# Performance work log

Hardware: AMD Instinct MI355X
Metric: run time of the kernel (lower is better)

Reference implementation:

```python
import jax, jax.numpy as jnp
import numpy as np

N_FREQS = 6  # PositionEmbedding N_freqs when embedding=='pe'

def _pe(x):
    freqs = (2.0 ** jnp.arange(N_FREQS)).astype(x.dtype)
    fx = x * freqs  # [B,Q,N_FREQS]
    sc = jnp.stack([jnp.sin(fx), jnp.cos(fx)], axis=-1).reshape(fx.shape[0], fx.shape[1], 2 * N_FREQS)
    return jnp.concatenate([x, sc], axis=-1)

def _mlp(h, W1, b1, W2, b2, W3, b3):
    h = jax.nn.relu(h @ W1 + b1)
    h = jax.nn.relu(h @ W2 + b2)
    return h @ W3 + b3

def setup_inputs() -> dict:
    key = jax.random.key(0)
    B, Q, N, D, H = 4, 65536, 8192, 16, 128
    ks = jax.random.split(key, 6)
    coord = jax.random.uniform(ks[0], (B, Q, 1), minval=-1.0, maxval=1.0, dtype=jnp.float32)
    latent = jax.random.normal(ks[1], (B, N, D), dtype=jnp.float32)
    in_dim = (1 + 2 * N_FREQS) + 3 * D  # pe(rel_coord) ++ unfolded feat = 13 + 48 = 61
    def init(k, shp, fan):
        return (jax.random.normal(k, shp, dtype=jnp.float32) / np.float32(np.sqrt(fan)))
    W1 = init(ks[2], (in_dim, H), in_dim); b1 = jnp.zeros((H,), jnp.float32)
    W2 = init(ks[3], (H, H), H);          b2 = jnp.zeros((H,), jnp.float32)
    W3 = init(ks[4], (H, 1), H);          b3 = jnp.zeros((1,), jnp.float32)
    return dict(coord=coord, latent=latent, W1=W1, b1=b1, W2=W2, b2=b2, W3=W3, b3=b3)

def reference(coord, latent, W1, b1, W2, b2, W3, b3):
    B, Q, _ = coord.shape
    N = latent.shape[1]
    # feat_unfold: concat shifted-prev / self / shifted-next along feature dim -> [B,N,3D]
    prev = jnp.concatenate([latent[:, :1], latent[:, :-1]], axis=1)
    nxt = jnp.concatenate([latent[:, 1:], latent[:, -1:]], axis=1)
    feat = jnp.concatenate([prev, latent, nxt], axis=-1)
    # make_coord grid: cell centers in [-1,1]
    grid = (-1.0 + (2.0 * jnp.arange(N, dtype=coord.dtype) + 1.0) / N)
    rx = 1.0 / N           # 2/num_latents/2
    eps_shift = 1e-6
    preds, areas = [], []
    for vx in (-2.0, 0.0):  # eval path vx_lst
        c = jnp.clip(coord + vx * rx + eps_shift, -1.0 + 1e-6, 1.0 - 1e-6)
        idx = jnp.clip(jnp.searchsorted(grid, c[..., 0]), 0, N - 1)  # [B,Q]
        q_coord = grid[idx][..., None]                               # [B,Q,1]
        q_feat = jnp.take_along_axis(feat, idx[..., None], axis=1)   # [B,Q,3D]
        rel = (coord - q_coord) * N                                  # scaled rel coord
        area = jnp.abs(rel[..., 0]) + 1e-9                           # [B,Q]
        inp = jnp.concatenate([_pe(rel), q_feat], axis=-1)           # [B,Q,61]
        preds.append(_mlp(inp, W1, b1, W2, b2, W3, b3))              # [B,Q,1]
        areas.append(area)
    tot = areas[0] + areas[1]
    # local_ensemble: swap areas before weighting
    ret = preds[0] * (areas[1] / tot)[..., None] + preds[1] * (areas[0] / tot)[..., None]
    return ret
```

## Files before the change

kernel.cpp:

```cpp
#include <hip/hip_runtime.h>
#include <hip/hip_bf16.h>

typedef short s8v __attribute__((ext_vector_type(8)));
typedef float f4v __attribute__((ext_vector_type(4)));

__device__ __forceinline__ unsigned short f2bf(float x) {
  unsigned u = __builtin_bit_cast(unsigned, x);
  u += 0x7fffu + ((u >> 16) & 1u);
  return (unsigned short)(u >> 16);
}
__device__ __forceinline__ unsigned pk2(float a, float b) {
  return (unsigned)f2bf(a) | ((unsigned)f2bf(b) << 16);
}

__global__ void prep_kernel(const float* __restrict__ W1, const float* __restrict__ b1,
                            const float* __restrict__ W2, unsigned short* __restrict__ wsW) {
  int e = blockIdx.x * 256 + threadIdx.x;
  if (e < 8192) {
    int frag = e >> 9, rem = e & 511, lane = rem >> 3, j = rem & 7;
    int h = frag >> 1, ks = frag & 1;
    int q4 = lane >> 4, l15 = lane & 15;
    int k = ks * 32 + q4 * 8 + j;
    int n = h * 16 + l15;
    float v;
    if (k < 13) v = W1[k * 128 + n];
    else if (k == 13) v = b1[n];
    else if (k < 16) v = 0.0f;
    else v = W1[(k - 3) * 128 + n];
    wsW[e] = f2bf(v);
  } else {
    int e2 = e - 8192;
    int frag = e2 >> 9, rem = e2 & 511, lane = rem >> 3, j = rem & 7;
    int h2 = frag >> 2, ks = frag & 3;
    int q4 = lane >> 4, l15 = lane & 15;
    int kd = (j < 4) ? (32 * ks + 4 * q4 + j) : (32 * ks + 16 + 4 * q4 + (j - 4));
    int n = h2 * 16 + l15;
    wsW[e] = f2bf(W2[kd * 128 + n]);
  }
}

__global__ __launch_bounds__(256, 2) void lisagon_main(
    const float* __restrict__ coord, const float* __restrict__ latent,
    const unsigned short* __restrict__ W1f, const unsigned short* __restrict__ W2f,
    const float* __restrict__ b2, const float* __restrict__ W3,
    const float* __restrict__ b3, float* __restrict__ out) {
  __shared__ __align__(16) unsigned short A1[256 * 64];
  __shared__ __align__(16) unsigned short W2s[16384];
  __shared__ float AREA[256];

  const int t = threadIdx.x;
  const int lane = t & 63, wv = t >> 6;
  const int l15 = lane & 15, q4 = lane >> 4;

  {
    const uint4* wsrc = (const uint4*)W2f;
    uint4* wdst = (uint4*)W2s;
#pragma unroll
    for (int it = 0; it < 8; it++) wdst[it * 256 + t] = wsrc[it * 256 + t];
  }

  {
    const int r = t;
    const int Rg = blockIdx.x * 256 + r;
    const int gq = Rg >> 1, p = Rg & 1;
    const float co = coord[gq];
    float c = (co + (p ? 0.0f : -0.000244140625f)) + 1e-6f;
    c = fminf(fmaxf(c, -1.0f + 1e-6f), 1.0f - 1e-6f);
    double u = ((double)c * 8192.0 + 8191.0) * 0.5;
    int idx = (int)ceil(u);
    idx = min(max(idx, 0), 8191);

    float qc = ((float)(2 * idx + 1) - 8192.0f) * (1.0f / 8192.0f);
    float rel = (co - qc) * 8192.0f;
    AREA[r] = fabsf(rel) + 1e-9f;

    uint4* A1v = (uint4*)A1;
    float v[16];
    v[0] = rel;
    float f = rel;
#pragma unroll
    for (int i = 0; i < 6; i++) {
      v[1 + 2 * i] = __sinf(f);
      v[2 + 2 * i] = __cosf(f);
      f = f + f;
    }
    v[13] = 1.0f;
    v[14] = 0.0f; v[15] = 0.0f;
#pragma unroll
    for (int ch = 0; ch < 2; ch++) {
      union { uint4 u4; unsigned us[4]; } pkv;
#pragma unroll
      for (int w = 0; w < 4; w++) pkv.us[w] = pk2(v[ch * 8 + 2 * w], v[ch * 8 + 2 * w + 1]);
      A1v[r * 8 + (ch ^ (r & 7))] = pkv.u4;
    }
    const float4* latv = (const float4*)(latent + (size_t)(gq >> 16) * (8192 * 16));
    int rows3[3];
    rows3[0] = max(idx - 1, 0);
    rows3[1] = idx;
    rows3[2] = min(idx + 1, 8191);
#pragma unroll
    for (int s = 0; s < 3; s++) {
      float4 a = latv[rows3[s] * 4 + 0];
      float4 b = latv[rows3[s] * 4 + 1];
      float4 cc = latv[rows3[s] * 4 + 2];
      float4 d = latv[rows3[s] * 4 + 3];
      union { uint4 u4; unsigned us[4]; } p0, p1;
      p0.us[0] = pk2(a.x, a.y); p0.us[1] = pk2(a.z, a.w);
      p0.us[2] = pk2(b.x, b.y); p0.us[3] = pk2(b.z, b.w);
      p1.us[0] = pk2(cc.x, cc.y); p1.us[1] = pk2(cc.z, cc.w);
      p1.us[2] = pk2(d.x, d.y);  p1.us[3] = pk2(d.z, d.w);
      int ch0 = 2 + 2 * s;
      A1v[r * 8 + (ch0 ^ (r & 7))]       = p0.u4;
      A1v[r * 8 + ((ch0 + 1) ^ (r & 7))] = p1.u4;
    }
  }
  __syncthreads();

  const s8v* W1fv = (const s8v*)W1f;
  const s8v* W2sv = (const s8v*)W2s;
  const s8v* A1s  = (const s8v*)A1;
  const int rbase = wv * 64;

  f4v acc1[8][4];
#pragma unroll
  for (int h = 0; h < 8; h++)
#pragma unroll
    for (int rt = 0; rt < 4; rt++) acc1[h][rt] = (f4v){0.f, 0.f, 0.f, 0.f};
#pragma unroll
  for (int ks = 0; ks < 2; ks++) {
    s8v Bf[4];
#pragma unroll
    for (int rt = 0; rt < 4; rt++) {
      int row = rbase + rt * 16 + l15;
      Bf[rt] = A1s[row * 8 + ((ks * 4 + q4) ^ (row & 7))];
    }
#pragma unroll
    for (int h = 0; h < 8; h++) {
      s8v Af = W1fv[(h * 2 + ks) * 64 + lane];
#pragma unroll
      for (int rt = 0; rt < 4; rt++)
        acc1[h][rt] = __builtin_amdgcn_mfma_f32_16x16x32_bf16(Af, Bf[rt], acc1[h][rt], 0, 0, 0);
    }
  }

  unsigned pk[4][8][2];
#pragma unroll
  for (int rt = 0; rt < 4; rt++)
#pragma unroll
    for (int h = 0; h < 8; h++) {
      pk[rt][h][0] = pk2(fmaxf(acc1[h][rt][0], 0.f), fmaxf(acc1[h][rt][1], 0.f));
      pk[rt][h][1] = pk2(fmaxf(acc1[h][rt][2], 0.f), fmaxf(acc1[h][rt][3], 0.f));
    }

  f4v acc2[8][4];
#pragma unroll
  for (int h2 = 0; h2 < 8; h2++)
#pragma unroll
    for (int rt = 0; rt < 4; rt++) acc2[h2][rt] = (f4v){0.f, 0.f, 0.f, 0.f};
#pragma unroll
  for (int ks = 0; ks < 4; ks++) {
    union { unsigned u[4]; s8v v; } bb[4];
#pragma unroll
    for (int rt = 0; rt < 4; rt++) {
      bb[rt].u[0] = pk[rt][2 * ks][0];     bb[rt].u[1] = pk[rt][2 * ks][1];
      bb[rt].u[2] = pk[rt][2 * ks + 1][0]; bb[rt].u[3] = pk[rt][2 * ks + 1][1];
    }
#pragma unroll
    for (int h2 = 0; h2 < 8; h2++) {
      s8v Af = W2sv[(h2 * 4 + ks) * 64 + lane];
#pragma unroll
      for (int rt = 0; rt < 4; rt++)
        acc2[h2][rt] = __builtin_amdgcn_mfma_f32_16x16x32_bf16(Af, bb[rt].v, acc2[h2][rt], 0, 0, 0);
    }
  }

  float s[4] = {0.f, 0.f, 0.f, 0.f};
#pragma unroll
  for (int h2 = 0; h2 < 8; h2++) {
    float4 b2v = ((const float4*)b2)[h2 * 4 + q4];
    float4 w3v = ((const float4*)W3)[h2 * 4 + q4];
#pragma unroll
    for (int rt = 0; rt < 4; rt++) {
      s[rt] += fmaxf(acc2[h2][rt][0] + b2v.x, 0.f) * w3v.x;
      s[rt] += fmaxf(acc2[h2][rt][1] + b2v.y, 0.f) * w3v.y;
      s[rt] += fmaxf(acc2[h2][rt][2] + b2v.z, 0.f) * w3v.z;
      s[rt] += fmaxf(acc2[h2][rt][3] + b2v.w, 0.f) * w3v.w;
    }
  }
  const float b3s = b3[0];
#pragma unroll
  for (int rt = 0; rt < 4; rt++) {
    float pred = s[rt];
    pred += __shfl_xor(pred, 16, 64);
    pred += __shfl_xor(pred, 32, 64);
    pred += b3s;
    float other = __shfl_xor(pred, 1, 64);
    if (q4 == 0 && (l15 & 1) == 0) {
      int row0 = rbase + rt * 16 + l15;
      float a0 = AREA[row0], a1 = AREA[row0 + 1];
      float tot = a0 + a1;
      out[(blockIdx.x * 256 + row0) >> 1] = pred * (a1 / tot) + other * (a0 / tot);
    }
  }
}

extern "C" void kernel_launch(void* const* d_in, const int* in_sizes, int n_in,
                              void* d_out, int out_size, void* d_ws, size_t ws_size,
                              hipStream_t stream) {
  const float* coord  = (const float*)d_in[0];
  const float* latent = (const float*)d_in[1];
  const float* W1 = (const float*)d_in[2];
  const float* b1 = (const float*)d_in[3];
  const float* W2 = (const float*)d_in[4];
  const float* b2 = (const float*)d_in[5];
  const float* W3 = (const float*)d_in[6];
  const float* b3 = (const float*)d_in[7];
  float* out = (float*)d_out;
  unsigned short* wsW = (unsigned short*)d_ws;

  prep_kernel<<<96, 256, 0, stream>>>(W1, b1, W2, wsW);
  lisagon_main<<<2048, 256, 0, stream>>>(coord, latent, wsW, wsW + 8192,
                                         b2, W3, b3, out);
}
```

Measured before the change: 109.1 us.

## Drop W2 LDS staging, raise occupancy, cheaper bf16 pack, hoist latent loads

Removes the per-block copy of W2 into shared memory and reads W2 fragments directly from global/L2, halving LDS use so launch bounds can request 4 blocks per SM. Replaces round-to-nearest-even bf16 conversion with a round-half-up add plus a byte-permute. Hoists the latent gathers ahead of the sin/cos computation so their latency overlaps, and folds b2 into the accumulator initialisation. Risks are register spills under the tighter launch bound, more global/L2 traffic for W2, and slightly different rounding.

```diff
diff --git a/kernel.cpp b/kernel.cpp
--- a/kernel.cpp
+++ b/kernel.cpp
@@ -10,7 +10,9 @@
   return (unsigned short)(u >> 16);
 }
 __device__ __forceinline__ unsigned pk2(float a, float b) {
-  return (unsigned)f2bf(a) | ((unsigned)f2bf(b) << 16);
+  unsigned ua = __builtin_bit_cast(unsigned, a) + 0x8000u;
+  unsigned ub = __builtin_bit_cast(unsigned, b) + 0x8000u;
+  return __builtin_amdgcn_perm(ub, ua, 0x07060302u);
 }
 
 __global__ void prep_kernel(const float* __restrict__ W1, const float* __restrict__ b1,
@@ -39,25 +41,17 @@
   }
 }
 
-__global__ __launch_bounds__(256, 2) void lisagon_main(
+__global__ __launch_bounds__(256, 4) void lisagon_main(
     const float* __restrict__ coord, const float* __restrict__ latent,
     const unsigned short* __restrict__ W1f, const unsigned short* __restrict__ W2f,
     const float* __restrict__ b2, const float* __restrict__ W3,
     const float* __restrict__ b3, float* __restrict__ out) {
   __shared__ __align__(16) unsigned short A1[256 * 64];
-  __shared__ __align__(16) unsigned short W2s[16384];
   __shared__ float AREA[256];
 
   const int t = threadIdx.x;
   const int lane = t & 63, wv = t >> 6;
   const int l15 = lane & 15, q4 = lane >> 4;
-
-  {
-    const uint4* wsrc = (const uint4*)W2f;
-    uint4* wdst = (uint4*)W2s;
-#pragma unroll
-    for (int it = 0; it < 8; it++) wdst[it * 256 + t] = wsrc[it * 256 + t];
-  }
 
   {
     const int r = t;
@@ -75,40 +69,42 @@
     AREA[r] = fabsf(rel) + 1e-9f;
 
     uint4* A1v = (uint4*)A1;
-    float v[16];
-    v[0] = rel;
-    float f = rel;
-#pragma unroll
-    for (int i = 0; i < 6; i++) {
-      v[1 + 2 * i] = __sinf(f);
-      v[2 + 2 * i] = __cosf(f);
-      f = f + f;
-    }
-    v[13] = 1.0f;
-    v[14] = 0.0f; v[15] = 0.0f;
-#pragma unroll
-    for (int ch = 0; ch < 2; ch++) {
-      union { uint4 u4; unsigned us[4]; } pkv;
-#pragma unroll
-      for (int w = 0; w < 4; w++) pkv.us[w] = pk2(v[ch * 8 + 2 * w], v[ch * 8 + 2 * w + 1]);
-      A1v[r * 8 + (ch ^ (r & 7))] = pkv.u4;
-    }
     const float4* latv = (const float4*)(latent + (size_t)(gq >> 16) * (8192 * 16));
     int rows3[3];
     rows3[0] = max(idx - 1, 0);
     rows3[1] = idx;
     rows3[2] = min(idx + 1, 8191);
+    float4 L[3][4];
+#pragma unroll
+    for (int s = 0; s < 3; s++)
+#pragma unroll
+      for (int w = 0; w < 4; w++) L[s][w] = latv[rows3[s] * 4 + w];
+
+    float v[16];
+    v[0] = rel;
+    float f = rel;
+#pragma unroll
+    for (int i = 0; i < 6; i++) {
+      v[1 + 2 * i] = __sinf(f);
+      v[2 + 2 * i] = __cosf(f);
+      f = f + f;
+    }
+    v[13] = 1.0f;
+    v[14] = 0.0f; v[15] = 0.0f;
+#pragma unroll
+    for (int ch = 0; ch < 2; ch++) {
+      union { uint4 u4; unsigned us[4]; } pkv;
+#pragma unroll
+      for (int w = 0; w < 4; w++) pkv.us[w] = pk2(v[ch * 8 + 2 * w], v[ch * 8 + 2 * w + 1]);
+      A1v[r * 8 + (ch ^ (r & 7))] = pkv.u4;
+    }
 #pragma unroll
     for (int s = 0; s < 3; s++) {
-      float4 a = latv[rows3[s] * 4 + 0];
-      float4 b = latv[rows3[s] * 4 + 1];
-      float4 cc = latv[rows3[s] * 4 + 2];
-      float4 d = latv[rows3[s] * 4 + 3];
       union { uint4 u4; unsigned us[4]; } p0, p1;
-      p0.us[0] = pk2(a.x, a.y); p0.us[1] = pk2(a.z, a.w);
-      p0.us[2] = pk2(b.x, b.y); p0.us[3] = pk2(b.z, b.w);
-      p1.us[0] = pk2(cc.x, cc.y); p1.us[1] = pk2(cc.z, cc.w);
-      p1.us[2] = pk2(d.x, d.y);  p1.us[3] = pk2(d.z, d.w);
+      p0.us[0] = pk2(L[s][0].x, L[s][0].y); p0.us[1] = pk2(L[s][0].z, L[s][0].w);
+      p0.us[2] = pk2(L[s][1].x, L[s][1].y); p0.us[3] = pk2(L[s][1].z, L[s][1].w);
+      p1.us[0] = pk2(L[s][2].x, L[s][2].y); p1.us[1] = pk2(L[s][2].z, L[s][2].w);
+      p1.us[2] = pk2(L[s][3].x, L[s][3].y); p1.us[3] = pk2(L[s][3].z, L[s][3].w);
       int ch0 = 2 + 2 * s;
       A1v[r * 8 + (ch0 ^ (r & 7))]       = p0.u4;
       A1v[r * 8 + ((ch0 + 1) ^ (r & 7))] = p1.u4;
@@ -117,7 +113,7 @@
   __syncthreads();
 
   const s8v* W1fv = (const s8v*)W1f;
-  const s8v* W2sv = (const s8v*)W2s;
+  const s8v* W2fv = (const s8v*)W2f;
   const s8v* A1s  = (const s8v*)A1;
   const int rbase = wv * 64;
 
@@ -154,9 +150,11 @@
 
   f4v acc2[8][4];
 #pragma unroll
-  for (int h2 = 0; h2 < 8; h2++)
-#pragma unroll
-    for (int rt = 0; rt < 4; rt++) acc2[h2][rt] = (f4v){0.f, 0.f, 0.f, 0.f};
+  for (int h2 = 0; h2 < 8; h2++) {
+    f4v b2v = ((const f4v*)b2)[h2 * 4 + q4];
+#pragma unroll
+    for (int rt = 0; rt < 4; rt++) acc2[h2][rt] = b2v;
+  }
 #pragma unroll
   for (int ks = 0; ks < 4; ks++) {
     union { unsigned u[4]; s8v v; } bb[4];
@@ -167,7 +165,7 @@
     }
 #pragma unroll
     for (int h2 = 0; h2 < 8; h2++) {
-      s8v Af = W2sv[(h2 * 4 + ks) * 64 + lane];
+      s8v Af = W2fv[(h2 * 4 + ks) * 64 + lane];
 #pragma unroll
       for (int rt = 0; rt < 4; rt++)
         acc2[h2][rt] = __builtin_amdgcn_mfma_f32_16x16x32_bf16(Af, bb[rt].v, acc2[h2][rt], 0, 0, 0);
@@ -177,14 +175,13 @@
   float s[4] = {0.f, 0.f, 0.f, 0.f};
 #pragma unroll
   for (int h2 = 0; h2 < 8; h2++) {
-    float4 b2v = ((const float4*)b2)[h2 * 4 + q4];
     float4 w3v = ((const float4*)W3)[h2 * 4 + q4];
 #pragma unroll
     for (int rt = 0; rt < 4; rt++) {
-      s[rt] += fmaxf(acc2[h2][rt][0] + b2v.x, 0.f) * w3v.x;
-      s[rt] += fmaxf(acc2[h2][rt][1] + b2v.y, 0.f) * w3v.y;
-      s[rt] += fmaxf(acc2[h2][rt][2] + b2v.z, 0.f) * w3v.z;
-      s[rt] += fmaxf(acc2[h2][rt][3] + b2v.w, 0.f) * w3v.w;
+      s[rt] += fmaxf(acc2[h2][rt][0], 0.f) * w3v.x;
+      s[rt] += fmaxf(acc2[h2][rt][1], 0.f) * w3v.y;
+      s[rt] += fmaxf(acc2[h2][rt][2], 0.f) * w3v.z;
+      s[rt] += fmaxf(acc2[h2][rt][3], 0.f) * w3v.w;
     }
   }
   const float b3s = b3[0];
```

After: 289.1 us. +165.0%, slower.
